# Optimization experiments

Measured on AMD Instinct MI355X. Metric: run time of the kernel, lower is better.

Reference implementation:

```python
import jax, jax.numpy as jnp
import numpy as np
from jax import lax

B, NODE, T, D_IN = 8, 1024, 12, 16
HID, GAT_OUT, PRED_LEN = 32, 32, 6
HEADS = 3
F_IN = HID * T      # 384
C = GAT_OUT * T     # 384
N = B * NODE        # 8192
E = 65536


def setup_inputs() -> dict:
    key = jax.random.key(0)
    ks = jax.random.split(key, 24)
    s = 0.05
    inp = {}
    inp["x"] = jax.random.normal(ks[0], (B, NODE, T, D_IN), jnp.float32)
    inp["edge_index"] = jax.random.randint(ks[1], (2, E), 0, N)
    inp["edge_attr"] = jax.random.normal(ks[2], (E, 1), jnp.float32)
    inp["batch_vec"] = jnp.repeat(jnp.arange(B), NODE)
    inp["alpha"] = 1.0
    # GRU params (torch gate order: r, z, n)
    inp["Wih"] = jax.random.normal(ks[3], (3 * HID, D_IN), jnp.float32) * s
    inp["Whh"] = jax.random.normal(ks[4], (3 * HID, HID), jnp.float32) * s
    inp["bih"] = jax.random.normal(ks[5], (3 * HID,), jnp.float32) * s
    inp["bhh"] = jax.random.normal(ks[6], (3 * HID,), jnp.float32) * s
    # GATConv params
    inp["Wgat"] = jax.random.normal(ks[7], (HEADS * C, F_IN), jnp.float32) * s
    inp["att_src"] = jax.random.normal(ks[8], (1, HEADS, C), jnp.float32) * s
    inp["att_dst"] = jax.random.normal(ks[9], (1, HEADS, C), jnp.float32) * s
    inp["Wedge"] = jax.random.normal(ks[10], (HEADS * C, 1), jnp.float32) * s
    inp["att_edge"] = jax.random.normal(ks[11], (1, HEADS, C), jnp.float32) * s
    inp["gat_bias"] = jax.random.normal(ks[12], (C,), jnp.float32) * s
    # predictors / classifiers
    inp["Wp1"] = jax.random.normal(ks[13], (1, GAT_OUT), jnp.float32) * s
    inp["bp1"] = jax.random.normal(ks[14], (1,), jnp.float32) * s
    inp["Wp3"] = jax.random.normal(ks[15], (PRED_LEN, T), jnp.float32) * s
    inp["bp3"] = jax.random.normal(ks[16], (PRED_LEN,), jnp.float32) * s
    inp["Wc1"] = jax.random.normal(ks[17], (GAT_OUT, T * GAT_OUT), jnp.float32) * s
    inp["bc1"] = jax.random.normal(ks[18], (GAT_OUT,), jnp.float32) * s
    inp["Wc2"] = jax.random.normal(ks[19], (2, GAT_OUT), jnp.float32) * s
    inp["bc2"] = jax.random.normal(ks[20], (2,), jnp.float32) * s
    return inp


def _gru(x, Wih, Whh, bih, bhh):
    # x: [rows, T, D_IN] -> [rows, T, HID]
    h0 = jnp.zeros((x.shape[0], HID), x.dtype)

    def step(h, xt):
        gi = xt @ Wih.T + bih
        gh = h @ Whh.T + bhh
        ir, iz, inn = jnp.split(gi, 3, axis=-1)
        hr, hz, hn = jnp.split(gh, 3, axis=-1)
        r = jax.nn.sigmoid(ir + hr)
        z = jax.nn.sigmoid(iz + hz)
        n = jnp.tanh(inn + r * hn)
        h_new = (1.0 - z) * n + z * h
        return h_new, h_new

    _, hs = lax.scan(step, h0, jnp.swapaxes(x, 0, 1))
    return jnp.swapaxes(hs, 0, 1)


def _gat(x, edge_index, edge_attr, Wgat, att_src, att_dst, Wedge, att_edge, bias):
    # PyG GATConv, heads=HEADS, concat=False, edge_dim=1, no self loops
    h = (x @ Wgat.T).reshape(N, HEADS, C)          # [N,H,C]
    a_src = (h * att_src).sum(-1)                  # [N,H]
    a_dst = (h * att_dst).sum(-1)                  # [N,H]
    src, dst = edge_index[0], edge_index[1]
    e = (edge_attr @ Wedge.T).reshape(-1, HEADS, C)
    a_edge = (e * att_edge).sum(-1)                # [E,H]
    a = jax.nn.leaky_relu(a_src[src] + a_dst[dst] + a_edge, 0.2)
    amax = jax.ops.segment_max(a, dst, num_segments=N)
    a = jnp.exp(a - amax[dst])
    denom = jax.ops.segment_sum(a, dst, num_segments=N)
    a = a / (denom[dst] + 1e-16)                   # segment softmax over incoming edges
    msg = h[src] * a[:, :, None]                   # [E,H,C]
    out = jax.ops.segment_sum(msg, dst, num_segments=N)
    return out.mean(axis=1) + bias                 # concat=False -> head mean


def reference(x, edge_index, edge_attr, batch_vec, alpha,
              Wih, Whh, bih, bhh,
              Wgat, att_src, att_dst, Wedge, att_edge, gat_bias,
              Wp1, bp1, Wp3, bp3, Wc1, bc1, Wc2, bc2):
    gru_in = x.reshape(-1, T, D_IN)                       # [N,T,D]
    gru_out = _gru(gru_in, Wih, Whh, bih, bhh)            # [N,T,HID]
    gat_in = gru_out.reshape(N, F_IN)
    gat_out = _gat(gat_in, edge_index, edge_attr, Wgat, att_src, att_dst,
                   Wedge, att_edge, gat_bias)             # [N,C]
    lin_in = gat_out.reshape(-1, T, GAT_OUT)              # [N,T,GAT_OUT]
    p = jax.nn.relu(jnp.einsum('ntc,oc->nto', lin_in, Wp1) + bp1).squeeze(-1)  # [N,T]
    p = jax.nn.relu(p @ Wp3.T + bp3)                      # [N,PRED_LEN]
    out_pred = p.reshape(B, NODE, PRED_LEN)
    # GRL is identity in forward
    pooled = jax.ops.segment_max(gat_out, batch_vec, num_segments=B)  # [B,C]
    l1 = pooled @ Wc1.T + bc1
    l2 = l1 @ Wc2.T + bc2
    out_label = jax.nn.softmax(l2, axis=1)
    return out_pred, out_label
```

## Files before the change

### kernel.cpp

```cpp
#include <hip/hip_runtime.h>
#include <hip/hip_bf16.h>

#define N_NODES 8192
#define E_EDGES 65536
#define HEADS 3
#define CDIM 384
#define NHC 1152
#define T_STEPS 12
#define D_IN 16
#define HID 32
#define PRED_LEN 6
#define OUT_LABEL_OFF 49152

#define O_X        0u
#define O_WIH      1572864u
#define O_WHH      1574400u
#define O_BIH      1577472u
#define O_BHH      1577568u
#define O_WGAT     1577664u
#define O_ATTS     2020032u
#define O_ATTD     2021184u
#define O_WEDGE    2022336u
#define O_ATTE     2023488u
#define O_GBIAS    2024640u
#define O_WP1      2025024u
#define O_BP1      2025056u
#define O_WP3      2025057u
#define O_BP3      2025129u
#define O_WC1      2025135u
#define O_BC1      2037423u
#define O_WC2      2037455u
#define O_BC2      2037519u
#define O_EATTR    2037521u
#define CONV_TOTAL 2103057u

#define O_GATIN    2103072u
#define O_GATB     O_GATIN
#define O_WGATB    (O_GATIN + 1572864u)
#define O_DEG      (O_GATIN + 1794048u)
#define O_ROWST    (O_GATIN + 1802240u)
#define O_CURS     (O_GATIN + 1810432u)
#define O_CSRE     (O_GATIN + 1818624u)
#define O_HFEAT    5248800u
#define O_ASRC     14685984u
#define O_ADST     14710560u
#define O_ARAW     14735136u
#define O_WEXP     14931744u
#define O_AMAX     15128352u
#define O_DENOM    15152928u
#define O_GMEAN    15177504u
#define O_POOLED   18323232u
#define O_KH       18326304u
#define O_FLAG     18326307u

typedef __attribute__((ext_vector_type(8))) short short8;
typedef __attribute__((ext_vector_type(4))) float floatx4;

__device__ __forceinline__ float b2f(unsigned short u) {
    return __uint_as_float(((unsigned)u) << 16);
}
__device__ __forceinline__ unsigned short f2b(float f) {
    __hip_bfloat16 b = __float2bfloat16(f);
    return *(unsigned short*)&b;
}
__device__ __forceinline__ unsigned enc_f(float f) {
    unsigned u = __float_as_uint(f);
    return (u & 0x80000000u) ? ~u : (u | 0x80000000u);
}
__device__ __forceinline__ float dec_f(unsigned e) {
    return __uint_as_float((e & 0x80000000u) ? (e & 0x7FFFFFFFu) : ~e);
}

__global__ __launch_bounds__(256) void fill_detect(
    const unsigned short* __restrict__ wih_raw,
    int* __restrict__ flag,
    float* __restrict__ W)
{
    if (blockIdx.x == 0 && threadIdx.x < 64) {
        int lane = threadIdx.x;
        int cnt = 0;
#pragma unroll
        for (int i = 0; i < 8; i++) {
            unsigned short h = wih_raw[(lane * 8 + i) * 2];
            int e = (h >> 7) & 0xFF;
            if (e >= 100 && e <= 127) cnt++;
        }
#pragma unroll
        for (int off = 32; off; off >>= 1) cnt += __shfl_down(cnt, off, 64);
        if (lane == 0) *flag = (cnt >= 300) ? 1 : 0;
    }
    unsigned idx = blockIdx.x * 256 + threadIdx.x;
    if      (idx < 24576u) W[O_AMAX  + idx] = 0.f;
    else if (idx < 49152u) W[O_DENOM + idx - 24576u] = 0.f;
    else if (idx < 52224u) W[O_POOLED + idx - 49152u] = 0.f;
    else if (idx < 60416u) ((int*)(W + O_DEG))[idx - 52224u] = 0;
}

__global__ __launch_bounds__(256) void convert_all(
    const int* __restrict__ flag,
    const void* x, const void* Wih, const void* Whh, const void* bih, const void* bhh,
    const void* Wgat, const void* atts, const void* attd, const void* Wedge, const void* atte,
    const void* gbias, const void* Wp1, const void* bp1, const void* Wp3, const void* bp3,
    const void* Wc1, const void* bc1, const void* Wc2, const void* bc2, const void* eattr,
    float* __restrict__ dst, unsigned short* __restrict__ wgatb)
{
    unsigned idx = blockIdx.x * 256 + threadIdx.x;
    if (idx >= CONV_TOTAL) return;
    if (idx >= O_WGAT && idx < O_ATTS) {
        unsigned off = idx - O_WGAT;
        wgatb[off] = (*flag) ? ((const unsigned short*)Wgat)[off]
                             : f2b(((const float*)Wgat)[off]);
        return;
    }
    const void* src; unsigned off;
    if      (idx < O_WIH)   { src = x;     off = idx - O_X; }
    else if (idx < O_WHH)   { src = Wih;   off = idx - O_WIH; }
    else if (idx < O_BIH)   { src = Whh;   off = idx - O_WHH; }
    else if (idx < O_BHH)   { src = bih;   off = idx - O_BIH; }
    else if (idx < O_WGAT)  { src = bhh;   off = idx - O_BHH; }
    else if (idx < O_ATTD)  { src = atts;  off = idx - O_ATTS; }
    else if (idx < O_WEDGE) { src = attd;  off = idx - O_ATTD; }
    else if (idx < O_ATTE)  { src = Wedge; off = idx - O_WEDGE; }
    else if (idx < O_GBIAS) { src = atte;  off = idx - O_ATTE; }
    else if (idx < O_WP1)   { src = gbias; off = idx - O_GBIAS; }
    else if (idx < O_BP1)   { src = Wp1;   off = idx - O_WP1; }
    else if (idx < O_BP3)   { src = (idx == O_BP1) ? bp1 : Wp3; off = (idx == O_BP1) ? 0 : idx - O_WP3; }
    else if (idx < O_WC1)   { src = bp3;   off = idx - O_BP3; }
    else if (idx < O_BC1)   { src = Wc1;   off = idx - O_WC1; }
    else if (idx < O_WC2)   { src = bc1;   off = idx - O_BC1; }
    else if (idx < O_BC2)   { src = Wc2;   off = idx - O_WC2; }
    else if (idx < O_EATTR) { src = bc2;   off = idx - O_BC2; }
    else                    { src = eattr; off = idx - O_EATTR; }
    float v = (*flag) ? b2f(((const unsigned short*)src)[off])
                      : ((const float*)src)[off];
    dst[idx] = v;
}

__global__ __launch_bounds__(256, 2) void gru_kernel(
    const float* __restrict__ xf,
    const float* __restrict__ Wih,
    const float* __restrict__ Whh,
    const float* __restrict__ bih,
    const float* __restrict__ bhh,
    unsigned short* __restrict__ gat_b)
{
    __shared__ float hsh[8][32];
    int gid = blockIdx.x * 256 + threadIdx.x;
    int n = gid >> 5;
    int j = gid & 31;
    int wid = threadIdx.x >> 5;

    float wih[3][16], whh[3][32], bi[3], bh[3];
#pragma unroll
    for (int g = 0; g < 3; g++) {
        int row = g * 32 + j;
#pragma unroll
        for (int i = 0; i < 16; i++) wih[g][i] = Wih[row * 16 + i];
#pragma unroll
        for (int i = 0; i < 32; i++) whh[g][i] = Whh[row * 32 + i];
        bi[g] = bih[row];
        bh[g] = bhh[row];
    }

    float hval = 0.f;
    hsh[wid][j] = 0.f;

    const float4* x4 = (const float4*)(xf + (size_t)n * 192);

    for (int t = 0; t < T_STEPS; t++) {
        float xv[16];
#pragma unroll
        for (int q = 0; q < 4; q++) {
            float4 p = x4[t * 4 + q];
            xv[q * 4 + 0] = p.x; xv[q * 4 + 1] = p.y;
            xv[q * 4 + 2] = p.z; xv[q * 4 + 3] = p.w;
        }

        float ir = bi[0], iz = bi[1], inn = bi[2];
#pragma unroll
        for (int i = 0; i < 16; i++) {
            ir  += wih[0][i] * xv[i];
            iz  += wih[1][i] * xv[i];
            inn += wih[2][i] * xv[i];
        }
        float hr = bh[0], hz = bh[1], hn = bh[2];
#pragma unroll
        for (int q = 0; q < 8; q++) {
            float4 hv = *(const float4*)&hsh[wid][q * 4];
            hr += whh[0][q*4+0]*hv.x + whh[0][q*4+1]*hv.y + whh[0][q*4+2]*hv.z + whh[0][q*4+3]*hv.w;
            hz += whh[1][q*4+0]*hv.x + whh[1][q*4+1]*hv.y + whh[1][q*4+2]*hv.z + whh[1][q*4+3]*hv.w;
            hn += whh[2][q*4+0]*hv.x + whh[2][q*4+1]*hv.y + whh[2][q*4+2]*hv.z + whh[2][q*4+3]*hv.w;
        }
        float r = 1.f / (1.f + expf(-(ir + hr)));
        float z = 1.f / (1.f + expf(-(iz + hz)));
        float nn = tanhf(inn + r * hn);
        hval = (1.f - z) * nn + z * hval;

        gat_b[(size_t)n * 384 + t * 32 + j] = f2b(hval);
        hsh[wid][j] = hval;
    }
}

__global__ __launch_bounds__(256) void gemm_mfma(
    const unsigned short* __restrict__ Ab,
    const unsigned short* __restrict__ Bb,
    unsigned short* __restrict__ Cb)
{
    __shared__ unsigned short sA[128][40];
    __shared__ unsigned short sB[128][40];
    int tid = threadIdx.x;
    int wave = tid >> 6, lane = tid & 63;
    int wm = (wave >> 1) * 64, wn = (wave & 1) * 64;
    int m0 = blockIdx.x * 128, n0 = blockIdx.y * 128;

    int r0 = tid >> 2;
    int c8 = (tid & 3) * 8;

    floatx4 acc[4][4];
#pragma unroll
    for (int i = 0; i < 4; i++)
#pragma unroll
        for (int j = 0; j < 4; j++) acc[i][j] = 0;

    int ml = lane & 15, kq = (lane >> 4) * 8;

    for (int k0 = 0; k0 < 384; k0 += 32) {
        short8 a0 = *(const short8*)(Ab + (size_t)(m0 + r0) * 384 + k0 + c8);
        short8 a1 = *(const short8*)(Ab + (size_t)(m0 + r0 + 64) * 384 + k0 + c8);
        short8 b0 = *(const short8*)(Bb + (size_t)(n0 + r0) * 384 + k0 + c8);
        short8 b1 = *(const short8*)(Bb + (size_t)(n0 + r0 + 64) * 384 + k0 + c8);

        __syncthreads();
        *(short8*)(&sA[r0][c8])      = a0;
        *(short8*)(&sA[r0 + 64][c8]) = a1;
        *(short8*)(&sB[r0][c8])      = b0;
        *(short8*)(&sB[r0 + 64][c8]) = b1;
        __syncthreads();

        short8 af[4], bf[4];
#pragma unroll
        for (int i = 0; i < 4; i++)
            af[i] = *(const short8*)(&sA[wm + i * 16 + ml][kq]);
#pragma unroll
        for (int j = 0; j < 4; j++)
            bf[j] = *(const short8*)(&sB[wn + j * 16 + ml][kq]);
#pragma unroll
        for (int i = 0; i < 4; i++)
#pragma unroll
            for (int j = 0; j < 4; j++)
                acc[i][j] = __builtin_amdgcn_mfma_f32_16x16x32_bf16(af[i], bf[j], acc[i][j], 0, 0, 0);
    }

    int cn = lane & 15, rq = (lane >> 4) * 4;
#pragma unroll
    for (int i = 0; i < 4; i++)
#pragma unroll
        for (int j = 0; j < 4; j++)
#pragma unroll
            for (int r = 0; r < 4; r++)
                Cb[(size_t)(m0 + wm + i * 16 + rq + r) * NHC + n0 + wn + j * 16 + cn] = f2b(acc[i][j][r]);
}

__global__ __launch_bounds__(256) void att_score_kernel(
    const unsigned short* __restrict__ h_bf,
    const float* __restrict__ att_src,
    const float* __restrict__ att_dst,
    const float* __restrict__ Wedge,
    const float* __restrict__ att_edge,
    float* __restrict__ a_src, float* __restrict__ a_dst,
    float* __restrict__ Kh)
{
    if (blockIdx.x == (N_NODES * 3) / 4) {
        if (threadIdx.x < 192) {
            int hd = threadIdx.x >> 6, lane = threadIdx.x & 63;
            float s = 0.f;
#pragma unroll
            for (int q = 0; q < 6; q++) {
                int c = lane + q * 64;
                s += Wedge[hd * CDIM + c] * att_edge[hd * CDIM + c];
            }
#pragma unroll
            for (int off = 32; off; off >>= 1) s += __shfl_down(s, off, 64);
            if (lane == 0) Kh[hd] = s;
        }
        return;
    }
    int w = (blockIdx.x * 256 + threadIdx.x) >> 6;
    int lane = threadIdx.x & 63;
    int n = w / 3, hd = w % 3;
    const unsigned short* hrow = h_bf + (size_t)n * NHC + hd * CDIM;
    float s0 = 0.f, s1 = 0.f;
#pragma unroll
    for (int q = 0; q < 6; q++) {
        int c = lane + q * 64;
        float hv = b2f(hrow[c]);
        s0 += hv * att_src[hd * CDIM + c];
        s1 += hv * att_dst[hd * CDIM + c];
    }
#pragma unroll
    for (int off = 32; off; off >>= 1) {
        s0 += __shfl_down(s0, off, 64);
        s1 += __shfl_down(s1, off, 64);
    }
    if (lane == 0) { a_src[n * 3 + hd] = s0; a_dst[n * 3 + hd] = s1; }
}

__global__ __launch_bounds__(256) void edge_score_kernel(
    const int* __restrict__ edge_index,
    const float* __restrict__ edge_attr,
    const float* __restrict__ a_src, const float* __restrict__ a_dst,
    const float* __restrict__ Kh,
    float* __restrict__ a_raw, unsigned* __restrict__ amax_enc,
    int* __restrict__ deg)
{
    int tid = blockIdx.x * 256 + threadIdx.x;
    int hd = tid >> 16;
    int e = tid & (E_EDGES - 1);
    int src = edge_index[e];
    int dst = edge_index[E_EDGES + e];
    float a = a_src[src * 3 + hd] + a_dst[dst * 3 + hd] + edge_attr[e] * Kh[hd];
    a = a > 0.f ? a : 0.2f * a;
    a_raw[hd * E_EDGES + e] = a;
    atomicMax(&amax_enc[dst * 3 + hd], enc_f(a));
    if (hd == 0) atomicAdd(&deg[dst], 1);
}

__global__ __launch_bounds__(256) void scan_kernel(
    const int* __restrict__ deg, int* __restrict__ rowstart, int* __restrict__ cursor)
{
    __shared__ int wtot[4];
    int t = threadIdx.x;
    int lane = t & 63, wv = t >> 6;
    int l[32], s = 0;
#pragma unroll
    for (int i = 0; i < 32; i++) { l[i] = deg[t * 32 + i]; s += l[i]; }
    int sc = s;
#pragma unroll
    for (int off = 1; off <= 32; off <<= 1) {
        int v = __shfl_up(sc, off, 64);
        if (lane >= off) sc += v;
    }
    if (lane == 63) wtot[wv] = sc;
    __syncthreads();
    int woff = 0;
#pragma unroll
    for (int w = 0; w < 4; w++) if (w < wv) woff += wtot[w];
    int b = woff + sc - s;
#pragma unroll
    for (int i = 0; i < 32; i++) {
        rowstart[t * 32 + i] = b;
        cursor[t * 32 + i] = b;
        b += l[i];
    }
}

__global__ __launch_bounds__(256) void edge_exp_kernel(
    const int* __restrict__ edge_index,
    const float* __restrict__ a_raw, const unsigned* __restrict__ amax_enc,
    float* __restrict__ w_exp, float* __restrict__ denom,
    int* __restrict__ cursor, int* __restrict__ csr_e)
{
    int tid = blockIdx.x * 256 + threadIdx.x;
    int hd = tid >> 16;
    int e = tid & (E_EDGES - 1);
    int dst = edge_index[E_EDGES + e];
    float m = dec_f(amax_enc[dst * 3 + hd]);
    float w = expf(a_raw[hd * E_EDGES + e] - m);
    w_exp[hd * E_EDGES + e] = w;
    unsafeAtomicAdd(&denom[dst * 3 + hd], w);
    if (hd == 0) {
        int pos = atomicAdd(&cursor[dst], 1);
        csr_e[pos] = e;
    }
}

__global__ __launch_bounds__(384) void aggregate_fused(
    const int* __restrict__ flag,
    const int* __restrict__ edge_index,
    const unsigned short* __restrict__ h_bf,
    const float* __restrict__ w_exp, const float* __restrict__ denom,
    const int* __restrict__ rowstart, const int* __restrict__ deg,
    const int* __restrict__ csr_e,
    const float* __restrict__ gat_bias,
    const float* __restrict__ Wp1, const float* __restrict__ bp1,
    const float* __restrict__ Wp3, const float* __restrict__ bp3,
    float* __restrict__ gmean,
    void* __restrict__ out_pred)
{
    int dst = blockIdx.x;
    int s = rowstart[dst], d = deg[dst];
    int tid = threadIdx.x;
    const float third = 1.f / 3.f;
    float inv0 = third / (denom[dst * 3 + 0] + 1e-16f);
    float inv1 = third / (denom[dst * 3 + 1] + 1e-16f);
    float inv2 = third / (denom[dst * 3 + 2] + 1e-16f);
    __shared__ int ssrc[64];
    __shared__ float sc0[64], sc1[64], sc2[64];
    __shared__ float gs[384];
    __shared__ float ps[12];
    float a = 0.f;
    for (int ch = 0; ch < d; ch += 64) {
        int m = d - ch; if (m > 64) m = 64;
        __syncthreads();
        if (tid < m) {
            int e = csr_e[s + ch + tid];
            ssrc[tid] = edge_index[e];
            sc0[tid] = w_exp[e] * inv0;
            sc1[tid] = w_exp[E_EDGES + e] * inv1;
            sc2[tid] = w_exp[2 * E_EDGES + e] * inv2;
        }
        __syncthreads();
        for (int i = 0; i < m; i++) {
            const unsigned short* hs = h_bf + (size_t)ssrc[i] * NHC;
            a += sc0[i] * b2f(hs[tid]) + sc1[i] * b2f(hs[tid + CDIM]) + sc2[i] * b2f(hs[tid + 2 * CDIM]);
        }
    }
    float g = a + gat_bias[tid];
    gmean[(size_t)dst * CDIM + tid] = g;
    gs[tid] = g;
    __syncthreads();

    int t = tid >> 5, c = tid & 31;
    float v = gs[t * 32 + c] * Wp1[c];
#pragma unroll
    for (int off = 16; off; off >>= 1) v += __shfl_down(v, off, 32);
    if (c == 0) { float p = v + bp1[0]; ps[t] = p > 0.f ? p : 0.f; }
    __syncthreads();

    if (tid < PRED_LEN) {
        float acc = bp3[tid];
#pragma unroll
        for (int tt = 0; tt < 12; tt++) acc += Wp3[tid * 12 + tt] * ps[tt];
        acc = acc > 0.f ? acc : 0.f;
        size_t oi = (size_t)dst * PRED_LEN + tid;
        if (*flag) ((__hip_bfloat16*)out_pred)[oi] = __float2bfloat16(acc);
        else       ((float*)out_pred)[oi] = acc;
    }
}

__global__ __launch_bounds__(384) void pool_kernel(
    const float* __restrict__ gmean,
    unsigned* __restrict__ pooled_enc)
{
    int b = blockIdx.x, ch = blockIdx.y;
    int tid = threadIdx.x;
    const float* base = gmean + ((size_t)b * 1024 + ch * 64) * CDIM + tid;
    float m = -3.4e38f;
    for (int i = 0; i < 64; i++)
        m = fmaxf(m, base[(size_t)i * CDIM]);
    atomicMax(&pooled_enc[b * CDIM + tid], enc_f(m));
}

__global__ __launch_bounds__(384) void cls_kernel(
    const int* __restrict__ flag,
    const unsigned* __restrict__ pooled_enc,
    const float* __restrict__ Wc1, const float* __restrict__ bc1,
    const float* __restrict__ Wc2, const float* __restrict__ bc2,
    void* __restrict__ out_base)
{
    int b = blockIdx.x, t = threadIdx.x;
    __shared__ float l1[32];
    if (t < 32) l1[t] = bc1[t];
    __syncthreads();
    float v = dec_f(pooled_enc[b * CDIM + t]);
#pragma unroll
    for (int i = 0; i < 32; i++) {
        float p = v * Wc1[i * CDIM + t];
#pragma unroll
        for (int off = 32; off; off >>= 1) p += __shfl_down(p, off, 64);
        if ((t & 63) == 0) atomicAdd(&l1[i], p);
    }
    __syncthreads();
    if (t == 0) {
        float l0 = bc2[0], l1v = bc2[1];
#pragma unroll
        for (int ii = 0; ii < 32; ii++) {
            l0  += Wc2[ii] * l1[ii];
            l1v += Wc2[32 + ii] * l1[ii];
        }
        float m = fmaxf(l0, l1v);
        float e0 = expf(l0 - m), e1 = expf(l1v - m);
        float s = e0 + e1;
        if (*flag) {
            __hip_bfloat16* ob = (__hip_bfloat16*)out_base;
            ob[OUT_LABEL_OFF + b * 2 + 0] = __float2bfloat16(e0 / s);
            ob[OUT_LABEL_OFF + b * 2 + 1] = __float2bfloat16(e1 / s);
        } else {
            float* of = (float*)out_base;
            of[OUT_LABEL_OFF + b * 2 + 0] = e0 / s;
            of[OUT_LABEL_OFF + b * 2 + 1] = e1 / s;
        }
    }
}

extern "C" void kernel_launch(void* const* d_in, const int* in_sizes, int n_in,
                              void* d_out, int out_size, void* d_ws, size_t ws_size,
                              hipStream_t stream) {
    float* W = (float*)d_ws;
    int* flag = (int*)(W + O_FLAG);
    const int* edge_index = (const int*)d_in[1];

    fill_detect<<<236, 256, 0, stream>>>(
        (const unsigned short*)d_in[5], flag, W);
    convert_all<<<(CONV_TOTAL + 255) / 256, 256, 0, stream>>>(
        flag,
        d_in[0], d_in[5], d_in[6], d_in[7], d_in[8],
        d_in[9], d_in[10], d_in[11], d_in[12], d_in[13],
        d_in[14], d_in[15], d_in[16], d_in[17], d_in[18],
        d_in[19], d_in[20], d_in[21], d_in[22], d_in[2],
        W, (unsigned short*)(W + O_WGATB));

    gru_kernel<<<N_NODES * 32 / 256, 256, 0, stream>>>(
        W + O_X, W + O_WIH, W + O_WHH, W + O_BIH, W + O_BHH,
        (unsigned short*)(W + O_GATB));
    gemm_mfma<<<dim3(N_NODES / 128, NHC / 128), 256, 0, stream>>>(
        (const unsigned short*)(W + O_GATB),
        (const unsigned short*)(W + O_WGATB),
        (unsigned short*)(W + O_HFEAT));
    att_score_kernel<<<(N_NODES * 3) / 4 + 1, 256, 0, stream>>>(
        (const unsigned short*)(W + O_HFEAT), W + O_ATTS, W + O_ATTD,
        W + O_WEDGE, W + O_ATTE,
        W + O_ASRC, W + O_ADST, W + O_KH);
    edge_score_kernel<<<3 * E_EDGES / 256, 256, 0, stream>>>(
        edge_index, W + O_EATTR, W + O_ASRC, W + O_ADST, W + O_KH,
        W + O_ARAW, (unsigned*)(W + O_AMAX), (int*)(W + O_DEG));
    scan_kernel<<<1, 256, 0, stream>>>(
        (const int*)(W + O_DEG), (int*)(W + O_ROWST), (int*)(W + O_CURS));
    edge_exp_kernel<<<3 * E_EDGES / 256, 256, 0, stream>>>(
        edge_index, W + O_ARAW, (const unsigned*)(W + O_AMAX),
        W + O_WEXP, W + O_DENOM, (int*)(W + O_CURS), (int*)(W + O_CSRE));
    aggregate_fused<<<N_NODES, 384, 0, stream>>>(
        flag, edge_index, (const unsigned short*)(W + O_HFEAT),
        W + O_WEXP, W + O_DENOM,
        (const int*)(W + O_ROWST), (const int*)(W + O_DEG),
        (const int*)(W + O_CSRE),
        W + O_GBIAS, W + O_WP1, W + O_BP1, W + O_WP3, W + O_BP3,
        W + O_GMEAN, d_out);
    pool_kernel<<<dim3(8, 16), 384, 0, stream>>>(
        W + O_GMEAN, (unsigned*)(W + O_POOLED));
    cls_kernel<<<8, 384, 0, stream>>>(
        flag, (const unsigned*)(W + O_POOLED),
        W + O_WC1, W + O_BC1, W + O_WC2, W + O_BC2, d_out);
}
```

Before: 274.1 us.

## Split GRU gates across threads with shared-memory staging and fast math

The GRU kernel now assigns one thread per (node, gate, hidden unit), using 96 threads per node and 4 nodes per 384-thread block, in place of one thread computing all three gates. The x sequence is staged in shared memory, and gate pre-activations are exchanged through shared arrays with two block barriers per timestep. Sigmoid and tanh switch to __expf plus hardware reciprocal. This cuts per-thread register pressure and serial FMA chains and raises thread-level parallelism. In exchange it adds 24 __syncthreads per block, leaves two thirds of the threads idle during the activation phase, and gives slightly less accurate transcendentals.

```diff
diff --git a/kernel.cpp b/kernel.cpp
--- a/kernel.cpp
+++ b/kernel.cpp
@@ -69,6 +69,9 @@
 }
 __device__ __forceinline__ float dec_f(unsigned e) {
     return __uint_as_float((e & 0x80000000u) ? (e & 0x7FFFFFFFu) : ~e);
+}
+__device__ __forceinline__ float fast_rcp(float x) {
+    return __builtin_amdgcn_rcpf(x);
 }
 
 __global__ __launch_bounds__(256) void fill_detect(
@@ -136,7 +139,8 @@
     dst[idx] = v;
 }
 
-__global__ __launch_bounds__(256, 2) void gru_kernel(
+#define GNODES 4
+__global__ __launch_bounds__(384) void gru_kernel(
     const float* __restrict__ xf,
     const float* __restrict__ Wih,
     const float* __restrict__ Whh,
@@ -144,60 +148,63 @@
     const float* __restrict__ bhh,
     unsigned short* __restrict__ gat_b)
 {
-    __shared__ float hsh[8][32];
-    int gid = blockIdx.x * 256 + threadIdx.x;
-    int n = gid >> 5;
-    int j = gid & 31;
-    int wid = threadIdx.x >> 5;
-
-    float wih[3][16], whh[3][32], bi[3], bh[3];
-#pragma unroll
-    for (int g = 0; g < 3; g++) {
-        int row = g * 32 + j;
-#pragma unroll
-        for (int i = 0; i < 16; i++) wih[g][i] = Wih[row * 16 + i];
-#pragma unroll
-        for (int i = 0; i < 32; i++) whh[g][i] = Whh[row * 32 + i];
-        bi[g] = bih[row];
-        bh[g] = bhh[row];
-    }
-
+    __shared__ float xsh[GNODES][192];
+    __shared__ float hsh[GNODES][32];
+    __shared__ float g0s[GNODES][32];
+    __shared__ float g1s[GNODES][32];
+    __shared__ float g2i[GNODES][32];
+    __shared__ float g2h[GNODES][32];
+
+    int tid = threadIdx.x;
+    int nl = tid / 96;
+    int r96 = tid - nl * 96;
+    int g = r96 >> 5, jj = r96 & 31;
+    int n = blockIdx.x * GNODES + nl;
+    int row = g * 32 + jj;
+
+    float wih[16], whh[32];
+#pragma unroll
+    for (int i = 0; i < 16; i++) wih[i] = Wih[row * 16 + i];
+#pragma unroll
+    for (int i = 0; i < 32; i++) whh[i] = Whh[row * 32 + i];
+    float bi = bih[row], bh = bhh[row];
+
+    const float* xrow = xf + (size_t)n * 192;
+    xsh[nl][r96]      = xrow[r96];
+    xsh[nl][r96 + 96] = xrow[r96 + 96];
+    if (g == 0) hsh[nl][jj] = 0.f;
     float hval = 0.f;
-    hsh[wid][j] = 0.f;
-
-    const float4* x4 = (const float4*)(xf + (size_t)n * 192);
+    __syncthreads();
 
     for (int t = 0; t < T_STEPS; t++) {
-        float xv[16];
+        float gi = bi;
 #pragma unroll
         for (int q = 0; q < 4; q++) {
-            float4 p = x4[t * 4 + q];
-            xv[q * 4 + 0] = p.x; xv[q * 4 + 1] = p.y;
-            xv[q * 4 + 2] = p.z; xv[q * 4 + 3] = p.w;
-        }
-
-        float ir = bi[0], iz = bi[1], inn = bi[2];
-#pragma unroll
-        for (int i = 0; i < 16; i++) {
-            ir  += wih[0][i] * xv[i];
-            iz  += wih[1][i] * xv[i];
-            inn += wih[2][i] * xv[i];
-        }
-        float hr = bh[0], hz = bh[1], hn = bh[2];
+            float4 xv = *(const float4*)&xsh[nl][t * 16 + q * 4];
+            gi += wih[q*4+0]*xv.x + wih[q*4+1]*xv.y + wih[q*4+2]*xv.z + wih[q*4+3]*xv.w;
+        }
+        float gh = bh;
 #pragma unroll
         for (int q = 0; q < 8; q++) {
-            float4 hv = *(const float4*)&hsh[wid][q * 4];
-            hr += whh[0][q*4+0]*hv.x + whh[0][q*4+1]*hv.y + whh[0][q*4+2]*hv.z + whh[0][q*4+3]*hv.w;
-            hz += whh[1][q*4+0]*hv.x + whh[1][q*4+1]*hv.y + whh[1][q*4+2]*hv.z + whh[1][q*4+3]*hv.w;
-            hn += whh[2][q*4+0]*hv.x + whh[2][q*4+1]*hv.y + whh[2][q*4+2]*hv.z + whh[2][q*4+3]*hv.w;
-        }
-        float r = 1.f / (1.f + expf(-(ir + hr)));
-        float z = 1.f / (1.f + expf(-(iz + hz)));
-        float nn = tanhf(inn + r * hn);
-        hval = (1.f - z) * nn + z * hval;
-
-        gat_b[(size_t)n * 384 + t * 32 + j] = f2b(hval);
-        hsh[wid][j] = hval;
+            float4 hv = *(const float4*)&hsh[nl][q * 4];
+            gh += whh[q*4+0]*hv.x + whh[q*4+1]*hv.y + whh[q*4+2]*hv.z + whh[q*4+3]*hv.w;
+        }
+        if (g == 0)      g0s[nl][jj] = gi + gh;
+        else if (g == 1) g1s[nl][jj] = gi + gh;
+        else             { g2i[nl][jj] = gi; g2h[nl][jj] = gh; }
+        __syncthreads();
+
+        if (g == 0) {
+            float r = fast_rcp(1.f + __expf(-g0s[nl][jj]));
+            float z = fast_rcp(1.f + __expf(-g1s[nl][jj]));
+            float pre = g2i[nl][jj] + r * g2h[nl][jj];
+            float e2 = __expf(2.f * pre);
+            float nn = 1.f - 2.f * fast_rcp(e2 + 1.f);
+            hval = (1.f - z) * nn + z * hval;
+            hsh[nl][jj] = hval;
+            gat_b[(size_t)n * 384 + t * 32 + jj] = f2b(hval);
+        }
+        __syncthreads();
     }
 }
 
@@ -510,7 +517,7 @@
         d_in[19], d_in[20], d_in[21], d_in[22], d_in[2],
         W, (unsigned short*)(W + O_WGATB));
 
-    gru_kernel<<<N_NODES * 32 / 256, 256, 0, stream>>>(
+    gru_kernel<<<N_NODES / GNODES, 384, 0, stream>>>(
         W + O_X, W + O_WIH, W + O_WHH, W + O_BIH, W + O_BHH,
         (unsigned short*)(W + O_GATB));
     gemm_mfma<<<dim3(N_NODES / 128, NHC / 128), 256, 0, stream>>>(
```

New measurement: 276.0 us. About the same (+0.7%).

## Rewrite GRU recurrence with bf16 MFMA over 16-node tiles

Applied to the files above, without the earlier changes.

The GRU kernel now processes 16 nodes per 64-thread wave, computing the input and hidden gate projections with 16x16x32 bf16 MFMA instructions instead of per-thread scalar FMAs held in large register arrays. Hidden state is exchanged through a small LDS buffer as bf16 fragments and written out with vectorized 16-byte stores. Gate nonlinearities use fast exp and reciprocal intrinsics in place of expf/tanhf. This cuts the FMA work and register pressure, but adds bf16 rounding of the weights, inputs and recurrent state, which lowers accuracy, and launches only 512 single-wave blocks.

```diff
diff --git a/kernel.cpp b/kernel.cpp
--- a/kernel.cpp
+++ b/kernel.cpp
@@ -63,12 +63,19 @@
     __hip_bfloat16 b = __float2bfloat16(f);
     return *(unsigned short*)&b;
 }
+__device__ __forceinline__ short f2bs(float f) {
+    __hip_bfloat16 b = __float2bfloat16(f);
+    return *(short*)&b;
+}
 __device__ __forceinline__ unsigned enc_f(float f) {
     unsigned u = __float_as_uint(f);
     return (u & 0x80000000u) ? ~u : (u | 0x80000000u);
 }
 __device__ __forceinline__ float dec_f(unsigned e) {
     return __uint_as_float((e & 0x80000000u) ? (e & 0x7FFFFFFFu) : ~e);
+}
+__device__ __forceinline__ float fast_rcp(float x) {
+    return __builtin_amdgcn_rcpf(x);
 }
 
 __global__ __launch_bounds__(256) void fill_detect(
@@ -136,68 +143,98 @@
     dst[idx] = v;
 }
 
-__global__ __launch_bounds__(256, 2) void gru_kernel(
-    const float* __restrict__ xf,
-    const float* __restrict__ Wih,
-    const float* __restrict__ Whh,
-    const float* __restrict__ bih,
-    const float* __restrict__ bhh,
+__global__ __launch_bounds__(64, 1) void gru_kernel(
+    const float* __restrict__ W,
     unsigned short* __restrict__ gat_b)
 {
-    __shared__ float hsh[8][32];
-    int gid = blockIdx.x * 256 + threadIdx.x;
-    int n = gid >> 5;
-    int j = gid & 31;
-    int wid = threadIdx.x >> 5;
-
-    float wih[3][16], whh[3][32], bi[3], bh[3];
-#pragma unroll
-    for (int g = 0; g < 3; g++) {
-        int row = g * 32 + j;
-#pragma unroll
-        for (int i = 0; i < 16; i++) wih[g][i] = Wih[row * 16 + i];
-#pragma unroll
-        for (int i = 0; i < 32; i++) whh[g][i] = Whh[row * 32 + i];
-        bi[g] = bih[row];
-        bh[g] = bhh[row];
-    }
-
-    float hval = 0.f;
-    hsh[wid][j] = 0.f;
-
-    const float4* x4 = (const float4*)(xf + (size_t)n * 192);
+    __shared__ short hbuf[16 * 40];
+    int lane = threadIdx.x;
+    int q = lane >> 4, nl = lane & 15;
+    int n0 = blockIdx.x * 16;
+    int n = n0 + nl;
+
+    const float* W_wih = W + O_WIH;
+    const float* W_whh = W + O_WHH;
+    const float* W_bih = W + O_BIH;
+    const float* W_bhh = W + O_BHH;
+    const float* W_x   = W + O_X;
+
+    short8 wh[6], wi[6];
+#pragma unroll
+    for (int c = 0; c < 6; c++) {
+        int row = c * 16 + nl;
+#pragma unroll
+        for (int r = 0; r < 8; r++) {
+            wh[c][r] = f2bs(W_whh[row * 32 + 8 * q + r]);
+            int k = 8 * q + r;
+            wi[c][r] = (k < 16) ? f2bs(W_wih[row * 16 + k]) : (short)0;
+        }
+    }
+    float br[8], bz[8], bni[8], bnh[8];
+#pragma unroll
+    for (int idx = 0; idx < 8; idx++) {
+        int c = idx >> 2, r = idx & 3;
+        int j = c * 16 + 4 * q + r;
+        br[idx]  = W_bih[j] + W_bhh[j];
+        bz[idx]  = W_bih[32 + j] + W_bhh[32 + j];
+        bni[idx] = W_bih[64 + j];
+        bnh[idx] = W_bhh[64 + j];
+    }
+
+    floatx4 zf = {0.f, 0.f, 0.f, 0.f};
+    short8 zs; 
+#pragma unroll
+    for (int r = 0; r < 8; r++) zs[r] = 0;
+
+    float hprev[8];
+#pragma unroll
+    for (int i = 0; i < 8; i++) hprev[i] = 0.f;
+    short8 hfrag = zs;
 
     for (int t = 0; t < T_STEPS; t++) {
-        float xv[16];
-#pragma unroll
-        for (int q = 0; q < 4; q++) {
-            float4 p = x4[t * 4 + q];
-            xv[q * 4 + 0] = p.x; xv[q * 4 + 1] = p.y;
-            xv[q * 4 + 2] = p.z; xv[q * 4 + 3] = p.w;
-        }
-
-        float ir = bi[0], iz = bi[1], inn = bi[2];
-#pragma unroll
-        for (int i = 0; i < 16; i++) {
-            ir  += wih[0][i] * xv[i];
-            iz  += wih[1][i] * xv[i];
-            inn += wih[2][i] * xv[i];
-        }
-        float hr = bh[0], hz = bh[1], hn = bh[2];
-#pragma unroll
-        for (int q = 0; q < 8; q++) {
-            float4 hv = *(const float4*)&hsh[wid][q * 4];
-            hr += whh[0][q*4+0]*hv.x + whh[0][q*4+1]*hv.y + whh[0][q*4+2]*hv.z + whh[0][q*4+3]*hv.w;
-            hz += whh[1][q*4+0]*hv.x + whh[1][q*4+1]*hv.y + whh[1][q*4+2]*hv.z + whh[1][q*4+3]*hv.w;
-            hn += whh[2][q*4+0]*hv.x + whh[2][q*4+1]*hv.y + whh[2][q*4+2]*hv.z + whh[2][q*4+3]*hv.w;
-        }
-        float r = 1.f / (1.f + expf(-(ir + hr)));
-        float z = 1.f / (1.f + expf(-(iz + hz)));
-        float nn = tanhf(inn + r * hn);
-        hval = (1.f - z) * nn + z * hval;
-
-        gat_b[(size_t)n * 384 + t * 32 + j] = f2b(hval);
-        hsh[wid][j] = hval;
+        short8 xf = zs;
+        if (q < 2) {
+            const float* xp = W_x + (size_t)n * 192 + t * 16 + 8 * q;
+            float4 xa = *(const float4*)xp;
+            float4 xb = *(const float4*)(xp + 4);
+            xf[0] = f2bs(xa.x); xf[1] = f2bs(xa.y); xf[2] = f2bs(xa.z); xf[3] = f2bs(xa.w);
+            xf[4] = f2bs(xb.x); xf[5] = f2bs(xb.y); xf[6] = f2bs(xb.z); xf[7] = f2bs(xb.w);
+        }
+
+        floatx4 aR0 = __builtin_amdgcn_mfma_f32_16x16x32_bf16(wi[0], xf, zf, 0, 0, 0);
+        aR0 = __builtin_amdgcn_mfma_f32_16x16x32_bf16(wh[0], hfrag, aR0, 0, 0, 0);
+        floatx4 aR1 = __builtin_amdgcn_mfma_f32_16x16x32_bf16(wi[1], xf, zf, 0, 0, 0);
+        aR1 = __builtin_amdgcn_mfma_f32_16x16x32_bf16(wh[1], hfrag, aR1, 0, 0, 0);
+        floatx4 aZ0 = __builtin_amdgcn_mfma_f32_16x16x32_bf16(wi[2], xf, zf, 0, 0, 0);
+        aZ0 = __builtin_amdgcn_mfma_f32_16x16x32_bf16(wh[2], hfrag, aZ0, 0, 0, 0);
+        floatx4 aZ1 = __builtin_amdgcn_mfma_f32_16x16x32_bf16(wi[3], xf, zf, 0, 0, 0);
+        aZ1 = __builtin_amdgcn_mfma_f32_16x16x32_bf16(wh[3], hfrag, aZ1, 0, 0, 0);
+        floatx4 aNI0 = __builtin_amdgcn_mfma_f32_16x16x32_bf16(wi[4], xf, zf, 0, 0, 0);
+        floatx4 aNI1 = __builtin_amdgcn_mfma_f32_16x16x32_bf16(wi[5], xf, zf, 0, 0, 0);
+        floatx4 aNH0 = __builtin_amdgcn_mfma_f32_16x16x32_bf16(wh[4], hfrag, zf, 0, 0, 0);
+        floatx4 aNH1 = __builtin_amdgcn_mfma_f32_16x16x32_bf16(wh[5], hfrag, zf, 0, 0, 0);
+
+#pragma unroll
+        for (int idx = 0; idx < 8; idx++) {
+            int c = idx >> 2, r = idx & 3;
+            float vR = (c ? aR1[r] : aR0[r]) + br[idx];
+            float vZ = (c ? aZ1[r] : aZ0[r]) + bz[idx];
+            float vNI = (c ? aNI1[r] : aNI0[r]) + bni[idx];
+            float vNH = (c ? aNH1[r] : aNH0[r]) + bnh[idx];
+            float rr = fast_rcp(1.f + __expf(-vR));
+            float zz = fast_rcp(1.f + __expf(-vZ));
+            float pre = vNI + rr * vNH;
+            float e2 = __expf(2.f * pre);
+            float nn = 1.f - 2.f * fast_rcp(e2 + 1.f);
+            float h = (1.f - zz) * nn + zz * hprev[idx];
+            hprev[idx] = h;
+            int j = c * 16 + 4 * q + r;
+            hbuf[nl * 40 + j] = f2bs(h);
+        }
+        hfrag = *(short8*)&hbuf[nl * 40 + 8 * q];
+        int sn = lane >> 2, jg = (lane & 3) * 8;
+        short8 hv = *(short8*)&hbuf[sn * 40 + jg];
+        *(short8*)(gat_b + (size_t)(n0 + sn) * 384 + t * 32 + jg) = hv;
     }
 }
 
@@ -275,8 +312,8 @@
             int hd = threadIdx.x >> 6, lane = threadIdx.x & 63;
             float s = 0.f;
 #pragma unroll
-            for (int q = 0; q < 6; q++) {
-                int c = lane + q * 64;
+            for (int qq = 0; qq < 6; qq++) {
+                int c = lane + qq * 64;
                 s += Wedge[hd * CDIM + c] * att_edge[hd * CDIM + c];
             }
 #pragma unroll
@@ -291,8 +328,8 @@
     const unsigned short* hrow = h_bf + (size_t)n * NHC + hd * CDIM;
     float s0 = 0.f, s1 = 0.f;
 #pragma unroll
-    for (int q = 0; q < 6; q++) {
-        int c = lane + q * 64;
+    for (int qq = 0; qq < 6; qq++) {
+        int c = lane + qq * 64;
         float hv = b2f(hrow[c]);
         s0 += hv * att_src[hd * CDIM + c];
         s1 += hv * att_dst[hd * CDIM + c];
@@ -510,9 +547,8 @@
         d_in[19], d_in[20], d_in[21], d_in[22], d_in[2],
         W, (unsigned short*)(W + O_WGATB));
 
-    gru_kernel<<<N_NODES * 32 / 256, 256, 0, stream>>>(
-        W + O_X, W + O_WIH, W + O_WHH, W + O_BIH, W + O_BHH,
-        (unsigned short*)(W + O_GATB));
+    gru_kernel<<<N_NODES / 16, 64, 0, stream>>>(
+        W, (unsigned short*)(W + O_GATB));
     gemm_mfma<<<dim3(N_NODES / 128, NHC / 128), 256, 0, stream>>>(
         (const unsigned short*)(W + O_GATB),
         (const unsigned short*)(W + O_WGATB),
```

After: 252.2 us. 8.0% less time.
